# Kernel tuning notes

Hardware: AMD Instinct MI355X
Metric: run time of the kernel (lower is better)

The kernel has to match this reference:

```python
import jax, jax.numpy as jnp
import numpy as np

B, Q, N, C = 16, 200, 200, 64   # batch, queries, candidates, edge classes
T = 100                          # matched targets per batch (len of prev_permutation_indices entries)
G, S = 50, 4                     # target groups per batch, edges per group (col_ids sizes)


def setup_inputs() -> dict:
    key = jax.random.key(0)
    k0, k1, k2, k3, k4 = jax.random.split(key, 5)
    batch_edges = jax.random.normal(k0, (B, Q, N, C), dtype=jnp.float32)
    query_indices = jax.random.randint(k1, (B, T), 0, N)           # index into N dim
    target_indices = jax.random.randint(k2, (B, T), 0, 10000)      # ordering keys, argsorted
    col_ids = jax.random.randint(k3, (B, G, S), 0, T)              # index into matched-target dim
    edge_target_indices = jax.random.randint(k4, (B, G, S), 0, C)  # class labels per edge
    return {
        "batch_edges": batch_edges,
        "query_indices": query_indices,
        "target_indices": target_indices,
        "col_ids": col_ids,
        "edge_target_indices": edge_target_indices,
    }


def reference(batch_edges, query_indices, target_indices, col_ids, edge_target_indices):
    # softmax over edge classes
    probs = jax.nn.softmax(batch_edges, axis=-1)                       # [B,Q,N,C]
    # sorted_query_indices = query_indices[argsort(target_indices)] per batch
    order = jnp.argsort(target_indices, axis=-1)                       # [B,T]
    sq = jnp.take_along_axis(query_indices, order, axis=-1)            # [B,T]
    # valid_edges = edges[:, prev_query_indices, :]
    valid = jnp.take_along_axis(probs, sq[:, None, :, None], axis=2)   # [B,Q,T,C]
    # all_edges = valid_edges[:, col_indices, :]  (col_ids flattened over groups)
    col_flat = col_ids.reshape(B, G * S)                               # [B,G*S]
    all_e = jnp.take_along_axis(valid, col_flat[:, None, :, None], axis=2)  # [B,Q,G*S,C]
    # pick target class per edge, negate, sum within each group
    tgt_flat = edge_target_indices.reshape(B, G * S)                   # [B,G*S]
    picked = jnp.take_along_axis(all_e, tgt_flat[:, None, :, None], axis=3)[..., 0]  # [B,Q,G*S]
    cost = -picked.reshape(B, Q, G, S).sum(axis=-1)                    # [B,Q,G]
    # torch.cat over batches along last dim -> [Q, B*G], then expand to [B,Q,B*G]
    cat = cost.transpose(1, 0, 2).reshape(Q, B * G)
    return jnp.broadcast_to(cat[None, :, :], (B, Q, B * G))
```

## Files before the change

### kernel.cpp

```cpp
#include <hip/hip_runtime.h>

#define BB 16
#define QQ 200
#define NN 200
#define CC 64
#define TT 100
#define GG 50
#define SS 4
#define EE (GG*SS)

__global__ __launch_bounds__(128) void precompute_sq_kernel(
    const int* __restrict__ query_indices,
    const int* __restrict__ target_indices,
    int* __restrict__ sq_out)
{
    const int b = blockIdx.x;
    __shared__ int tk[TT];
    __shared__ int qi[TT];
    __shared__ int sq_sh[TT];
    const int tid = threadIdx.x;
    if (tid < TT) {
        tk[tid] = target_indices[b * TT + tid];
        qi[tid] = query_indices[b * TT + tid];
    }
    __syncthreads();
    if (tid < TT) {
        const int key = tk[tid];
        int rank = 0;
        #pragma unroll 4
        for (int j = 0; j < TT; ++j) {
            const int kj = tk[j];
            rank += (kj < key) || (kj == key && j < tid);
        }
        sq_sh[rank] = qi[tid];
    }
    __syncthreads();
    if (tid < TT) sq_out[b * TT + tid] = sq_sh[tid];
}

__global__ __launch_bounds__(256) void edge_cost_kernel(
    const float* __restrict__ edges,
    const int* __restrict__ sq,
    const int* __restrict__ col_ids,
    const int* __restrict__ tgt,
    float* __restrict__ out)
{
    const int blk = blockIdx.x;
    const int b = blk / QQ;
    const int q = blk % QQ;
    const int tid = threadIdx.x;

    __shared__ int   sq_sh[TT];
    __shared__ float mx_sh[TT];
    __shared__ float sm_sh[TT];
    __shared__ float cost_sh[GG];

    if (tid < TT) sq_sh[tid] = sq[b * TT + tid];
    __syncthreads();

    const float* base = edges + ((size_t)(b * QQ + q)) * NN * CC;

    const int grp  = tid >> 4;
    const int lane = tid & 15;
    for (int t = grp; t < TT; t += 16) {
        const float4 v = reinterpret_cast<const float4*>(base + (size_t)sq_sh[t] * CC)[lane];
        float m = fmaxf(fmaxf(v.x, v.y), fmaxf(v.z, v.w));
        #pragma unroll
        for (int off = 1; off < 16; off <<= 1)
            m = fmaxf(m, __shfl_xor(m, off, 64));
        float e = __expf(v.x - m) + __expf(v.y - m) + __expf(v.z - m) + __expf(v.w - m);
        #pragma unroll
        for (int off = 1; off < 16; off <<= 1)
            e += __shfl_xor(e, off, 64);
        if (lane == 0) { mx_sh[t] = m; sm_sh[t] = e; }
    }
    __syncthreads();

    if (tid < EE) {
        const int t_e = col_ids[b * EE + tid];
        const int c_e = tgt[b * EE + tid];
        const float x = base[(size_t)sq_sh[t_e] * CC + c_e];
        float p = __expf(x - mx_sh[t_e]) / sm_sh[t_e];
        p += __shfl_xor(p, 1, 64);
        p += __shfl_xor(p, 2, 64);
        if ((tid & 3) == 0) cost_sh[tid >> 2] = -p;
    }
    __syncthreads();

    for (int i = tid; i < BB * GG; i += 256) {
        const int b2 = i / GG;
        const int g  = i % GG;
        out[((size_t)b2 * QQ + q) * (BB * GG) + b * GG + g] = cost_sh[g];
    }
}

extern "C" void kernel_launch(void* const* d_in, const int* in_sizes, int n_in,
                              void* d_out, int out_size, void* d_ws, size_t ws_size,
                              hipStream_t stream) {
    const float* edges = (const float*)d_in[0];
    const int* query_indices  = (const int*)d_in[1];
    const int* target_indices = (const int*)d_in[2];
    const int* col_ids        = (const int*)d_in[3];
    const int* edge_tgt       = (const int*)d_in[4];
    float* out = (float*)d_out;
    int* sq_ws = (int*)d_ws;

    precompute_sq_kernel<<<BB, 128, 0, stream>>>(query_indices, target_indices, sq_ws);
    edge_cost_kernel<<<BB * QQ, 256, 0, stream>>>(edges, sq_ws, col_ids, edge_tgt, out);
}
```

Measured before the change: 27.65 us.

## Skip unused target rows, drop softmax max, process two queries per block

Precompute kernel now compacts the list of target rows actually referenced by col_ids and packs per-edge (row,class) indices. The edge kernel computes softmax denominators only for those rows, omits the max-subtraction, and handles two queries per block to amortize index loading. Removing the max subtraction risks overflow for large logits and the serial compaction on one thread adds small precompute latency.

New measurement: 35.19 us. 27.3% more time.

```diff
diff --git a/kernel.cpp b/kernel.cpp
--- a/kernel.cpp
+++ b/kernel.cpp
@@ -8,20 +8,26 @@
 #define GG 50
 #define SS 4
 #define EE (GG*SS)
+#define QPB 2
 
-__global__ __launch_bounds__(128) void precompute_sq_kernel(
+__global__ __launch_bounds__(128) void precompute_kernel(
     const int* __restrict__ query_indices,
     const int* __restrict__ target_indices,
-    int* __restrict__ sq_out)
+    const int* __restrict__ col_ids,
+    const int* __restrict__ edge_tgt,
+    int* __restrict__ n_list,
+    int* __restrict__ cnt_out,
+    int* __restrict__ edge_pack)
 {
     const int b = blockIdx.x;
-    __shared__ int tk[TT];
-    __shared__ int qi[TT];
-    __shared__ int sq_sh[TT];
     const int tid = threadIdx.x;
+    __shared__ int tk[TT], qi[TT], sq_sh[TT];
+    __shared__ int used[TT], uidx[TT];
+
     if (tid < TT) {
         tk[tid] = target_indices[b * TT + tid];
         qi[tid] = query_indices[b * TT + tid];
+        used[tid] = 0;
     }
     __syncthreads();
     if (tid < TT) {
@@ -35,62 +41,89 @@
         sq_sh[rank] = qi[tid];
     }
     __syncthreads();
-    if (tid < TT) sq_out[b * TT + tid] = sq_sh[tid];
+    for (int e = tid; e < EE; e += 128)
+        used[col_ids[b * EE + e]] = 1;
+    __syncthreads();
+    if (tid == 0) {
+        int c = 0;
+        for (int t = 0; t < TT; ++t) {
+            if (used[t]) { uidx[t] = c; n_list[b * TT + c] = sq_sh[t]; ++c; }
+        }
+        cnt_out[b] = c;
+    }
+    __syncthreads();
+    for (int e = tid; e < EE; e += 128) {
+        const int t = col_ids[b * EE + e];
+        const int c = edge_tgt[b * EE + e];
+        edge_pack[b * EE + e] = uidx[t] * 64 + c;
+    }
 }
 
 __global__ __launch_bounds__(256) void edge_cost_kernel(
     const float* __restrict__ edges,
-    const int* __restrict__ sq,
-    const int* __restrict__ col_ids,
-    const int* __restrict__ tgt,
+    const int* __restrict__ n_list,
+    const int* __restrict__ cnt_in,
+    const int* __restrict__ edge_pack,
     float* __restrict__ out)
 {
     const int blk = blockIdx.x;
-    const int b = blk / QQ;
-    const int q = blk % QQ;
+    const int b = blk / (QQ / QPB);
+    const int q0 = (blk % (QQ / QPB)) * QPB;
     const int tid = threadIdx.x;
 
-    __shared__ int   sq_sh[TT];
-    __shared__ float mx_sh[TT];
-    __shared__ float sm_sh[TT];
-    __shared__ float cost_sh[GG];
+    __shared__ int   n_sh[TT];
+    __shared__ int   ep_sh[EE];
+    __shared__ float sm_sh[QPB][TT];
+    __shared__ float cost_sh[QPB][GG];
+    __shared__ int   cnt_sh;
 
-    if (tid < TT) sq_sh[tid] = sq[b * TT + tid];
+    if (tid == 0) cnt_sh = cnt_in[b];
+    if (tid < TT) n_sh[tid] = n_list[b * TT + tid];
+    if (tid < EE) ep_sh[tid] = edge_pack[b * EE + tid];
     __syncthreads();
 
-    const float* base = edges + ((size_t)(b * QQ + q)) * NN * CC;
+    const int cnt = cnt_sh;
+    const float* base = edges + ((size_t)(b * QQ + q0)) * NN * CC;
 
     const int grp  = tid >> 4;
     const int lane = tid & 15;
-    for (int t = grp; t < TT; t += 16) {
-        const float4 v = reinterpret_cast<const float4*>(base + (size_t)sq_sh[t] * CC)[lane];
-        float m = fmaxf(fmaxf(v.x, v.y), fmaxf(v.z, v.w));
+    for (int t = grp; t < cnt; t += 16) {
+        const float* r0 = base + (size_t)n_sh[t] * CC;
+        const float4 v0 = reinterpret_cast<const float4*>(r0)[lane];
+        const float4 v1 = reinterpret_cast<const float4*>(r0 + NN * CC)[lane];
+        float e0 = __expf(v0.x) + __expf(v0.y) + __expf(v0.z) + __expf(v0.w);
+        float e1 = __expf(v1.x) + __expf(v1.y) + __expf(v1.z) + __expf(v1.w);
         #pragma unroll
-        for (int off = 1; off < 16; off <<= 1)
-            m = fmaxf(m, __shfl_xor(m, off, 64));
-        float e = __expf(v.x - m) + __expf(v.y - m) + __expf(v.z - m) + __expf(v.w - m);
-        #pragma unroll
-        for (int off = 1; off < 16; off <<= 1)
-            e += __shfl_xor(e, off, 64);
-        if (lane == 0) { mx_sh[t] = m; sm_sh[t] = e; }
+        for (int off = 1; off < 16; off <<= 1) {
+            e0 += __shfl_xor(e0, off, 64);
+            e1 += __shfl_xor(e1, off, 64);
+        }
+        if (lane == 0) { sm_sh[0][t] = e0; sm_sh[1][t] = e1; }
     }
     __syncthreads();
 
     if (tid < EE) {
-        const int t_e = col_ids[b * EE + tid];
-        const int c_e = tgt[b * EE + tid];
-        const float x = base[(size_t)sq_sh[t_e] * CC + c_e];
-        float p = __expf(x - mx_sh[t_e]) / sm_sh[t_e];
-        p += __shfl_xor(p, 1, 64);
-        p += __shfl_xor(p, 2, 64);
-        if ((tid & 3) == 0) cost_sh[tid >> 2] = -p;
+        const int pack = ep_sh[tid];
+        const int u = pack >> 6;
+        const int c = pack & 63;
+        const size_t roff = (size_t)n_sh[u] * CC + c;
+        #pragma unroll
+        for (int qq = 0; qq < QPB; ++qq) {
+            const float x = base[(size_t)qq * NN * CC + roff];
+            float p = __expf(x) / sm_sh[qq][u];
+            p += __shfl_xor(p, 1, 64);
+            p += __shfl_xor(p, 2, 64);
+            if ((tid & 3) == 0) cost_sh[qq][tid >> 2] = -p;
+        }
     }
     __syncthreads();
 
-    for (int i = tid; i < BB * GG; i += 256) {
-        const int b2 = i / GG;
-        const int g  = i % GG;
-        out[((size_t)b2 * QQ + q) * (BB * GG) + b * GG + g] = cost_sh[g];
+    for (int i = tid; i < QPB * BB * GG; i += 256) {
+        const int qq = i / (BB * GG);
+        const int r  = i % (BB * GG);
+        const int b2 = r / GG;
+        const int g  = r % GG;
+        out[((size_t)b2 * QQ + q0 + qq) * (BB * GG) + b * GG + g] = cost_sh[qq][g];
     }
 }
 
@@ -103,8 +136,14 @@
     const int* col_ids        = (const int*)d_in[3];
     const int* edge_tgt       = (const int*)d_in[4];
     float* out = (float*)d_out;
-    int* sq_ws = (int*)d_ws;
 
-    precompute_sq_kernel<<<BB, 128, 0, stream>>>(query_indices, target_indices, sq_ws);
-    edge_cost_kernel<<<BB * QQ, 256, 0, stream>>>(edges, sq_ws, col_ids, edge_tgt, out);
+    int* n_list    = (int*)d_ws;
+    int* cnt_ws    = n_list + BB * TT;
+    int* edge_pack = cnt_ws + BB;
+
+    precompute_kernel<<<BB, 128, 0, stream>>>(query_indices, target_indices,
+                                              col_ids, edge_tgt,
+                                              n_list, cnt_ws, edge_pack);
+    edge_cost_kernel<<<BB * (QQ / QPB), 256, 0, stream>>>(edges, n_list, cnt_ws,
+                                                          edge_pack, out);
 }
```

## Deduplicate gathered rows and precompute packed edge indices; drop softmax max subtraction

Applied to the files above, without the earlier changes.

The precompute kernel now finds the set of distinct candidate rows actually referenced by edges, emits a compact row list and count, and packs each edge's slot and class into one integer. The main kernel reduces only those unique rows and reads the packed indices from shared memory, avoiding loads of unreferenced rows and per-edge index lookups. The softmax no longer subtracts the row maximum, which saves a shuffle reduction but risks overflow for large logits. The dedup uses a serial single-thread scan in the precompute kernel.

New measurement: 39.45 us. 1.43x slower.

```diff
diff --git a/kernel.cpp b/kernel.cpp
--- a/kernel.cpp
+++ b/kernel.cpp
@@ -9,20 +9,26 @@
 #define SS 4
 #define EE (GG*SS)
 
-__global__ __launch_bounds__(128) void precompute_sq_kernel(
+__global__ __launch_bounds__(256) void precompute_kernel(
     const int* __restrict__ query_indices,
     const int* __restrict__ target_indices,
-    int* __restrict__ sq_out)
+    const int* __restrict__ col_ids,
+    const int* __restrict__ edge_tgt,
+    int* __restrict__ n_list,
+    int* __restrict__ cnt_out,
+    int* __restrict__ edge_pack)
 {
     const int b = blockIdx.x;
-    __shared__ int tk[TT];
-    __shared__ int qi[TT];
-    __shared__ int sq_sh[TT];
     const int tid = threadIdx.x;
+    __shared__ int tk[TT], qi[TT], sq_sh[TT];
+    __shared__ int used[NN];
+    __shared__ int slot[NN];
+
     if (tid < TT) {
         tk[tid] = target_indices[b * TT + tid];
         qi[tid] = query_indices[b * TT + tid];
     }
+    if (tid < NN) used[tid] = 0;
     __syncthreads();
     if (tid < TT) {
         const int key = tk[tid];
@@ -35,14 +41,28 @@
         sq_sh[rank] = qi[tid];
     }
     __syncthreads();
-    if (tid < TT) sq_out[b * TT + tid] = sq_sh[tid];
+    if (tid < EE) used[sq_sh[col_ids[b * EE + tid]]] = 1;
+    __syncthreads();
+    if (tid == 0) {
+        int c = 0;
+        for (int n = 0; n < NN; ++n) {
+            if (used[n]) { slot[n] = c; n_list[b * TT + c] = n; ++c; }
+        }
+        cnt_out[b] = c;
+    }
+    __syncthreads();
+    if (tid < EE) {
+        const int n = sq_sh[col_ids[b * EE + tid]];
+        const int c = edge_tgt[b * EE + tid];
+        edge_pack[b * EE + tid] = slot[n] * 64 + c;
+    }
 }
 
 __global__ __launch_bounds__(256) void edge_cost_kernel(
     const float* __restrict__ edges,
-    const int* __restrict__ sq,
-    const int* __restrict__ col_ids,
-    const int* __restrict__ tgt,
+    const int* __restrict__ n_list,
+    const int* __restrict__ cnt_in,
+    const int* __restrict__ edge_pack,
     float* __restrict__ out)
 {
     const int blk = blockIdx.x;
@@ -50,37 +70,36 @@
     const int q = blk % QQ;
     const int tid = threadIdx.x;
 
-    __shared__ int   sq_sh[TT];
-    __shared__ float mx_sh[TT];
+    __shared__ int   n_sh[TT];
+    __shared__ int   ep_sh[EE];
     __shared__ float sm_sh[TT];
     __shared__ float cost_sh[GG];
 
-    if (tid < TT) sq_sh[tid] = sq[b * TT + tid];
+    const int cnt = cnt_in[b];
+    if (tid < cnt) n_sh[tid] = n_list[b * TT + tid];
+    if (tid < EE) ep_sh[tid] = edge_pack[b * EE + tid];
     __syncthreads();
 
     const float* base = edges + ((size_t)(b * QQ + q)) * NN * CC;
 
     const int grp  = tid >> 4;
     const int lane = tid & 15;
-    for (int t = grp; t < TT; t += 16) {
-        const float4 v = reinterpret_cast<const float4*>(base + (size_t)sq_sh[t] * CC)[lane];
-        float m = fmaxf(fmaxf(v.x, v.y), fmaxf(v.z, v.w));
-        #pragma unroll
-        for (int off = 1; off < 16; off <<= 1)
-            m = fmaxf(m, __shfl_xor(m, off, 64));
-        float e = __expf(v.x - m) + __expf(v.y - m) + __expf(v.z - m) + __expf(v.w - m);
+    for (int t = grp; t < cnt; t += 16) {
+        const float4 v = reinterpret_cast<const float4*>(base + (size_t)n_sh[t] * CC)[lane];
+        float e = __expf(v.x) + __expf(v.y) + __expf(v.z) + __expf(v.w);
         #pragma unroll
         for (int off = 1; off < 16; off <<= 1)
             e += __shfl_xor(e, off, 64);
-        if (lane == 0) { mx_sh[t] = m; sm_sh[t] = e; }
+        if (lane == 0) sm_sh[t] = e;
     }
     __syncthreads();
 
     if (tid < EE) {
-        const int t_e = col_ids[b * EE + tid];
-        const int c_e = tgt[b * EE + tid];
-        const float x = base[(size_t)sq_sh[t_e] * CC + c_e];
-        float p = __expf(x - mx_sh[t_e]) / sm_sh[t_e];
+        const int pack = ep_sh[tid];
+        const int u = pack >> 6;
+        const int c = pack & 63;
+        const float x = base[(size_t)n_sh[u] * CC + c];
+        float p = __expf(x) / sm_sh[u];
         p += __shfl_xor(p, 1, 64);
         p += __shfl_xor(p, 2, 64);
         if ((tid & 3) == 0) cost_sh[tid >> 2] = -p;
@@ -103,8 +122,14 @@
     const int* col_ids        = (const int*)d_in[3];
     const int* edge_tgt       = (const int*)d_in[4];
     float* out = (float*)d_out;
-    int* sq_ws = (int*)d_ws;
 
-    precompute_sq_kernel<<<BB, 128, 0, stream>>>(query_indices, target_indices, sq_ws);
-    edge_cost_kernel<<<BB * QQ, 256, 0, stream>>>(edges, sq_ws, col_ids, edge_tgt, out);
+    int* n_list    = (int*)d_ws;
+    int* cnt_ws    = n_list + BB * TT;
+    int* edge_pack = cnt_ws + BB;
+
+    precompute_kernel<<<BB, 256, 0, stream>>>(query_indices, target_indices,
+                                              col_ids, edge_tgt,
+                                              n_list, cnt_ws, edge_pack);
+    edge_cost_kernel<<<BB * QQ, 256, 0, stream>>>(edges, n_list, cnt_ws,
+                                                  edge_pack, out);
 }
```
